# Performance work log

Measured on AMD Instinct MI355X. Metric: run time of the kernel, lower is better.

Reference implementation:

```python
import jax, jax.numpy as jnp
import numpy as np

NUM_ROUTES = 32 * 6 * 6  # 1152
NUM_CAPS = 10
IN_DIM = 8
OUT_DIM = 16
NUM_ITERS = 3

def _conv(x, w, stride):
    return jax.lax.conv_general_dilated(
        x, w, window_strides=(stride, stride), padding='VALID',
        dimension_numbers=('NCHW', 'OIHW', 'NCHW'))

def _squash(u):
    # squash over last axis, exactly as torch code (no eps)
    sn = (u ** 2).sum(-1, keepdims=True)
    return sn * u / ((1.0 + sn) * jnp.sqrt(sn))

def setup_inputs() -> dict:
    key = jax.random.key(0)
    ks = jax.random.split(key, 10)
    B = 512
    data = jax.random.normal(ks[0], (B, 1, 28, 28), dtype=jnp.float32)
    conv_w = jax.random.normal(ks[1], (256, 1, 9, 9), dtype=jnp.float32) * 0.05
    conv_b = jnp.zeros((256,), dtype=jnp.float32)
    # 8 primary-capsule convs stacked caps-major -> fused conv [8*32,256,9,9]
    pc_w = jax.random.normal(ks[2], (8 * 32, 256, 9, 9), dtype=jnp.float32) * 0.01
    pc_b = jnp.zeros((8 * 32,), dtype=jnp.float32)
    W = jax.random.normal(ks[3], (NUM_ROUTES, NUM_CAPS, OUT_DIM, IN_DIM), dtype=jnp.float32)
    enc_w1 = jax.random.normal(ks[4], (512, OUT_DIM * NUM_CAPS), dtype=jnp.float32) * 0.05
    enc_b1 = jnp.zeros((512,), dtype=jnp.float32)
    enc_w2 = jax.random.normal(ks[5], (9, 512), dtype=jnp.float32) * 0.05
    enc_b2 = jnp.zeros((9,), dtype=jnp.float32)
    return dict(data=data, conv_w=conv_w, conv_b=conv_b, pc_w=pc_w, pc_b=pc_b,
                W=W, enc_w1=enc_w1, enc_b1=enc_b1, enc_w2=enc_w2, enc_b2=enc_b2)

def reference(data, conv_w, conv_b, pc_w, pc_b, W, enc_w1, enc_b1, enc_w2, enc_b2):
    B = data.shape[0]
    # ConvLayer: conv + relu -> [B,256,20,20]
    x = jax.nn.relu(_conv(data, conv_w, 1) + conv_b[None, :, None, None])
    # PrimaryCaps: 8 stride-2 convs (fused, caps-major channels) -> [B,256,6,6]
    u = _conv(x, pc_w, 2) + pc_b[None, :, None, None]
    # torch: stack(dim=1) then view(B, num_routes, -1) == reshape caps-major flat
    u = u.reshape(B, NUM_ROUTES, IN_DIM)
    u = _squash(u)  # [B,R,8]
    # WaferCaps: u_hat[b,r,c,o] = sum_i W[r,c,o,i] * u[b,r,i]
    u_hat = jnp.einsum('rcoi,bri->brco', W, u)  # [B,R,C,O]
    b_ij = jnp.zeros((NUM_ROUTES, NUM_CAPS), dtype=u_hat.dtype)
    v = None
    for it in range(NUM_ITERS):
        c_ij = jax.nn.softmax(b_ij, axis=0)  # softmax over routes (dim=1 in torch)
        s = jnp.einsum('rc,brco->bco', c_ij, u_hat)  # [B,C,O]
        # original squashes [B,1,C,O,1] over last (size-1) dim -> elementwise
        s2 = s ** 2
        v = s2 * s / ((1.0 + s2) * jnp.sqrt(s2))  # = s*|s|/(1+s^2)
        if it < NUM_ITERS - 1:
            a = jnp.einsum('brco,bco->brc', u_hat, v)  # [B,R,C]
            b_ij = b_ij + a.mean(axis=0)
    # Encoder: flatten [B,C,O] row-major -> [B,160]
    flat = v.reshape(B, NUM_CAPS * OUT_DIM)
    h = jax.nn.relu(flat @ enc_w1.T + enc_b1)  # dropout is identity at eval
    out = jax.nn.sigmoid(h @ enc_w2.T + enc_b2)
    return out
```

## Files before the change

kernel.cpp:

```cpp
#include <hip/hip_runtime.h>
#include <hip/hip_bf16.h>
#include <stdint.h>


typedef __bf16 bf16_t;
typedef __bf16 bf16x4 __attribute__((ext_vector_type(4)));
typedef __bf16 bf16x8 __attribute__((ext_vector_type(8)));
typedef float f32x4 __attribute__((ext_vector_type(4)));
typedef int i32x4 __attribute__((ext_vector_type(4)));
typedef int i32x8 __attribute__((ext_vector_type(8)));

__device__ __forceinline__ void gload_lds16(const void* g, void* l) {
    __builtin_amdgcn_global_load_lds((const __attribute__((address_space(1))) void*)g,
                                     (__attribute__((address_space(3))) void*)l, 16, 0, 0);
}

#define MEMBAR() asm volatile("" ::: "memory")

__device__ __forceinline__ uint8_t fp8b(float v) {
    return (uint8_t)(__builtin_amdgcn_cvt_pk_fp8_f32(v, 0.f, 0, false) & 0xFF);
}

__global__ void k_prep(const float* __restrict__ w1, const float* __restrict__ cw,
                       float* __restrict__ w1t, bf16_t* __restrict__ Bc1,
                       float* __restrict__ bij) {
    int blk = blockIdx.x, tid = threadIdx.x;
    if (blk < 45) {
        int i = blk * 256 + tid;
        if (i < 11520) bij[i] = 0.f;
    } else if (blk < 365) {
        int i = (blk - 45) * 256 + tid;
        int j = i / 160, k = i % 160;
        w1t[k * 512 + j] = w1[i];
    } else {
        int i = (blk - 365) * 256 + tid;
        if (i < 26624) {
            int oc = i / 104, k = i % 104;
            Bc1[i] = (k < 81) ? (bf16_t)cw[oc * 81 + k] : (bf16_t)0.f;
        }
    }
}

__global__ __launch_bounds__(256) void k_w2t(const float* __restrict__ pcw,
                                             uint8_t* __restrict__ w2t8) {
    __shared__ uint16_t tmp16[10368];
    int oc = blockIdx.x, tid = threadIdx.x;
    const float* src = pcw + (size_t)oc * 20736;
    for (int q2 = tid; q2 < 10368; q2 += 256) {
        float a = src[q2 * 2] * 64.f;
        float b = src[q2 * 2 + 1] * 64.f;
        uint32_t pk = __builtin_amdgcn_cvt_pk_fp8_f32(a, b, 0, false);
        tmp16[q2] = (uint16_t)(pk & 0xFFFF);
    }
    __syncthreads();
    uint32_t* dst = (uint32_t*)(w2t8 + (size_t)oc * 20736);
    for (int w = tid; w < 5184; w += 256) {
        int k = w * 4;
        int t = k >> 8, ic0 = k & 255;
        uint32_t r = 0;
#pragma unroll
        for (int j = 0; j < 4; ++j) {
            int s = (ic0 + j) * 81 + t;
            uint32_t b = (tmp16[s >> 1] >> ((s & 1) * 8)) & 0xFF;
            r |= b << (8 * j);
        }
        dst[w] = r;
    }
}

__global__ __launch_bounds__(512) void k_c1gemm(const float* __restrict__ data,
                                                const bf16_t* __restrict__ Bc1,
                                                const float* __restrict__ cb,
                                                uint8_t* __restrict__ xt8) {
    __shared__ __align__(16) bf16_t As[128 * 104];
    __shared__ __align__(16) bf16_t Bs[256 * 104];
    int tid = threadIdx.x, lane = tid & 63, wave = tid >> 6;
    int wm = wave >> 2, wn = wave & 3;
    for (int i = tid; i < 3328; i += 512) {
        int byte = i * 16;
        int r = byte / 208;
        int c16 = (byte - r * 208) >> 4;
        gload_lds16(Bc1 + r * 104 + c16 * 8, (char*)Bs + byte);
    }
    int mr = wm * 64 + (lane & 15);
    int nr = wn * 64 + (lane & 15);
    float bias[4];
#pragma unroll
    for (int nj = 0; nj < 4; ++nj) bias[nj] = cb[nr + nj * 16];

    for (int t = 0; t < 2; ++t) {
        int m0 = (blockIdx.x + t * 800) * 128;
        __syncthreads();
        for (int z = tid; z < 128 * 23; z += 512) {
            int r = z / 23, k = 81 + z - (z / 23) * 23;
            As[r * 104 + k] = (bf16_t)0.f;
        }
        for (int pr = tid; pr < 1152; pr += 512) {
            int r = pr / 9, kh = pr - (pr / 9) * 9;
            int m = m0 + r;
            int b = m / 400, pos = m - b * 400;
            int oh = pos / 20, ow = pos - oh * 20;
            const float* src = data + (size_t)b * 784 + (oh + kh) * 28 + ow;
            bf16_t* dst = &As[r * 104 + kh * 9];
#pragma unroll
            for (int j = 0; j < 9; ++j) dst[j] = (bf16_t)src[j];
        }
        asm volatile("s_waitcnt vmcnt(0)" ::: "memory");
        __syncthreads();
        f32x4 acc[4][4];
#pragma unroll
        for (int mi = 0; mi < 4; ++mi)
#pragma unroll
            for (int nj = 0; nj < 4; ++nj) acc[mi][nj] = (f32x4){0.f, 0.f, 0.f, 0.f};
#pragma unroll
        for (int kk = 0; kk < 3; ++kk) {
            int ch = (kk * 4 + (lane >> 4)) * 8;
            bf16x8 af[4], bfr[4];
#pragma unroll
            for (int i = 0; i < 4; ++i) af[i] = *(const bf16x8*)&As[(mr + i * 16) * 104 + ch];
#pragma unroll
            for (int j = 0; j < 4; ++j) bfr[j] = *(const bf16x8*)&Bs[(nr + j * 16) * 104 + ch];
#pragma unroll
            for (int mi = 0; mi < 4; ++mi)
#pragma unroll
                for (int nj = 0; nj < 4; ++nj)
                    acc[mi][nj] = __builtin_amdgcn_mfma_f32_16x16x32_bf16(af[mi], bfr[nj], acc[mi][nj], 0, 0, 0);
        }
        int mbase = m0 + wm * 64 + (lane >> 4) * 4;
#pragma unroll
        for (int mi = 0; mi < 4; ++mi)
#pragma unroll
            for (int nj = 0; nj < 4; ++nj)
#pragma unroll
                for (int j = 0; j < 4; ++j)
                    xt8[(size_t)(mbase + mi * 16 + j) * 256 + nr + nj * 16] =
                        fp8b(fmaxf(acc[mi][nj][j] + bias[nj], 0.f));
    }
}

__global__ __launch_bounds__(256) void k_pcgemm(const uint8_t* __restrict__ xt8,
                                                const uint8_t* __restrict__ w2t8,
                                                bf16_t* __restrict__ parts) {
    __shared__ __align__(16) uint8_t As[128 * 128];
    __shared__ __align__(16) uint8_t Bs[128 * 128];
    int bid = blockIdx.x;
    int mt = bid % 144;
    int nt = (bid / 144) & 1;
    int ks = bid / 288;
    int m0 = mt * 128, n0 = nt * 128;
    int tid = threadIdx.x, lane = tid & 63, wave = tid >> 6;

    int csrc = (tid & 7) ^ ((tid >> 3) & 7);
    int arow[4];
#pragma unroll
    for (int p = 0; p < 4; ++p) {
        int m = m0 + p * 32 + (tid >> 3);
        int bb = m / 36, pos = m % 36;
        int oh = pos / 6, ow = pos % 6;
        arow[p] = ((bb * 20 + oh * 2) * 20 + ow * 2) * 256;
    }
    const uint8_t* bbase = w2t8 + (size_t)(n0 + (tid >> 3)) * 20736 + csrc * 16;

    f32x4 acc[4][4];
#pragma unroll
    for (int mi = 0; mi < 4; ++mi)
#pragma unroll
        for (int ni = 0; ni < 4; ++ni) acc[mi][ni] = (f32x4){0.f, 0.f, 0.f, 0.f};

    int g0 = ks * 81;
    int mr = (wave >> 1) * 64 + (lane & 15);
    int nr = (wave & 1) * 64 + (lane & 15);
    int rx = lane & 7;
    int c0 = (2 * (lane >> 4)) ^ rx;
    int c1 = (2 * (lane >> 4) + 1) ^ rx;

    for (int it = 0; it < 81; ++it) {
        int g = g0 + it;
        int t = g >> 1, icb = g & 1;
        int kh = t / 9, kw = t - (t / 9) * 9;
        int aoff = (kh * 20 + kw) * 256 + icb * 128 + csrc * 16;
#pragma unroll
        for (int p = 0; p < 4; ++p) {
            gload_lds16(xt8 + arow[p] + aoff, &As[p * 4096 + tid * 16]);
            gload_lds16(bbase + (size_t)p * 32 * 20736 + (size_t)g * 128, &Bs[p * 4096 + tid * 16]);
        }
        __syncthreads();
        i32x8 af[4], bfr[4];
#pragma unroll
        for (int i = 0; i < 4; ++i) {
            i32x4 lo = *(const i32x4*)&As[(mr + i * 16) * 128 + c0 * 16];
            i32x4 hi = *(const i32x4*)&As[(mr + i * 16) * 128 + c1 * 16];
            af[i][0] = lo[0]; af[i][1] = lo[1]; af[i][2] = lo[2]; af[i][3] = lo[3];
            af[i][4] = hi[0]; af[i][5] = hi[1]; af[i][6] = hi[2]; af[i][7] = hi[3];
        }
#pragma unroll
        for (int i = 0; i < 4; ++i) {
            i32x4 lo = *(const i32x4*)&Bs[(nr + i * 16) * 128 + c0 * 16];
            i32x4 hi = *(const i32x4*)&Bs[(nr + i * 16) * 128 + c1 * 16];
            bfr[i][0] = lo[0]; bfr[i][1] = lo[1]; bfr[i][2] = lo[2]; bfr[i][3] = lo[3];
            bfr[i][4] = hi[0]; bfr[i][5] = hi[1]; bfr[i][6] = hi[2]; bfr[i][7] = hi[3];
        }
#pragma unroll
        for (int mi = 0; mi < 4; ++mi)
#pragma unroll
            for (int ni = 0; ni < 4; ++ni)
                acc[mi][ni] = __builtin_amdgcn_mfma_scale_f32_16x16x128_f8f6f4(
                    af[mi], bfr[ni], acc[mi][ni], 0, 0, 0, 0x7F7F7F7F, 0, 0x79797979);
        __syncthreads();
    }

    bf16_t* out = parts + (size_t)ks * 4718592;
    int mbase = m0 + (wave >> 1) * 64 + (lane >> 4) * 4;
    int nbase = n0 + (wave & 1) * 64 + (lane & 15);
#pragma unroll
    for (int mi = 0; mi < 4; ++mi)
#pragma unroll
        for (int ni = 0; ni < 4; ++ni)
#pragma unroll
            for (int j = 0; j < 4; ++j)
                out[(size_t)(mbase + mi * 16 + j) * 256 + nbase + ni * 16] = (bf16_t)acc[mi][ni][j];
}

__global__ __launch_bounds__(256) void k_squash(const bf16_t* __restrict__ parts,
                                                const float* __restrict__ pcb,
                                                bf16_t* __restrict__ ub) {
    __shared__ float s[36 * 257];
    int b = blockIdx.x, tid = threadIdx.x;
    for (int i = tid; i < 9216; i += 256) {
        float a = pcb[i & 255];
#pragma unroll
        for (int p = 0; p < 2; ++p) a += (float)parts[(size_t)p * 4718592 + (size_t)b * 9216 + i];
        s[(i >> 8) * 257 + (i & 255)] = a;
    }
    __syncthreads();
    for (int r = tid; r < 1152; r += 256) {
        int flat0 = r * 8;
        float val[8], sn = 0.f;
#pragma unroll
        for (int e = 0; e < 8; ++e) {
            int f = flat0 + e;
            float x = s[(f % 36) * 257 + f / 36];
            val[e] = x;
            sn += x * x;
        }
        float scale = sn / ((1.f + sn) * sqrtf(sn));
        bf16x8 vv;
#pragma unroll
        for (int e = 0; e < 8; ++e) vv[e] = (bf16_t)(val[e] * scale);
        *(bf16x8*)&ub[(size_t)b * 9216 + flat0] = vv;
    }
}

__global__ __launch_bounds__(256) void k_uT(const bf16_t* __restrict__ ub, bf16_t* __restrict__ uT) {
    __shared__ bf16_t t[64 * 66];
    int kt = blockIdx.x % 144, bt = blockIdx.x / 144;
    int k0 = kt * 64, b0 = bt * 64;
    int tid = threadIdx.x;
    int c8 = tid & 7;
#pragma unroll
    for (int p = 0; p < 2; ++p) {
        int r = p * 32 + (tid >> 3);
        bf16x8 vv = *(const bf16x8*)&ub[(size_t)(b0 + r) * 9216 + k0 + c8 * 8];
        uint32_t u4[4];
        *(bf16x8*)u4 = vv;
#pragma unroll
        for (int j2 = 0; j2 < 4; ++j2)
            *(uint32_t*)&t[r * 66 + c8 * 8 + j2 * 2] = u4[j2];
    }
    __syncthreads();
#pragma unroll
    for (int p = 0; p < 2; ++p) {
        int kp = p * 32 + (tid >> 3);
        bf16x8 vv;
#pragma unroll
        for (int j = 0; j < 8; ++j) vv[j] = t[(c8 * 8 + j) * 66 + kp];
        *(bf16x8*)&uT[(size_t)(k0 + kp) * 512 + b0 + c8 * 8] = vv;
    }
}

__global__ void k_cij(const float* __restrict__ bij, float* __restrict__ cij) {
    __shared__ float red[256];
    int c = blockIdx.x, tid = threadIdx.x;
    float mx = -1e30f;
    for (int r = tid; r < 1152; r += 256) mx = fmaxf(mx, bij[r * 10 + c]);
    red[tid] = mx; __syncthreads();
    for (int s = 128; s > 0; s >>= 1) { if (tid < s) red[tid] = fmaxf(red[tid], red[tid + s]); __syncthreads(); }
    float MX = red[0]; __syncthreads();
    float sm = 0.f;
    for (int r = tid; r < 1152; r += 256) sm += expf(bij[r * 10 + c] - MX);
    red[tid] = sm; __syncthreads();
    for (int s = 128; s > 0; s >>= 1) { if (tid < s) red[tid] += red[tid + s]; __syncthreads(); }
    float inv = 1.f / red[0];
    for (int r = tid; r < 1152; r += 256) cij[r * 10 + c] = expf(bij[r * 10 + c] - MX) * inv;
}

__global__ void k_fold(const float* __restrict__ cij, const float* __restrict__ W,
                       bf16_t* __restrict__ cw2T) {
    int idx = blockIdx.x * 256 + threadIdx.x;
    int co = idx / 9216, k = idx % 9216;
    int r = k >> 3, i = k & 7;
    int c = co >> 4, o = co & 15;
    cw2T[idx] = (bf16_t)(cij[r * 10 + c] * W[((size_t)(r * 10 + c) * 16 + o) * 8 + i]);
}

__global__ void k_fold0(const float* __restrict__ W, bf16_t* __restrict__ cw2T) {
    int idx = blockIdx.x * 256 + threadIdx.x;
    int co = idx / 9216, k = idx % 9216;
    int r = k >> 3, i = k & 7;
    int c = co >> 4, o = co & 15;
    cw2T[idx] = (bf16_t)(W[((size_t)(r * 10 + c) * 16 + o) * 8 + i] * (1.0f / 1152.0f));
}

__global__ __launch_bounds__(256) void k_rgemm(const bf16_t* __restrict__ A,
                                               const bf16_t* __restrict__ B,
                                               bf16_t* __restrict__ Cp,
                                               int Kfull, int steps, int mtiles) {
    __shared__ __align__(16) bf16_t As[64 * 64];
    __shared__ __align__(16) bf16_t Bs[160 * 64];
    int bid = blockIdx.x;
    int mt = bid % mtiles, ks = bid / mtiles;
    int m0 = mt * 64;
    int k0 = ks * steps * 64;
    int tid = threadIdx.x, lane = tid & 63, wave = tid >> 6;
    int srow = tid >> 3;
    int csrc = (tid & 7) ^ (srow & 7);
    const bf16_t* asrc[2];
    const bf16_t* bsrc[5];
#pragma unroll
    for (int p = 0; p < 2; ++p)
        asrc[p] = A + (size_t)(m0 + p * 32 + srow) * Kfull + k0 + csrc * 8;
#pragma unroll
    for (int p = 0; p < 5; ++p)
        bsrc[p] = B + (size_t)(p * 32 + srow) * Kfull + k0 + csrc * 8;

    f32x4 acc[2][5];
#pragma unroll
    for (int mi = 0; mi < 2; ++mi)
#pragma unroll
        for (int nj = 0; nj < 5; ++nj) acc[mi][nj] = (f32x4){0.f, 0.f, 0.f, 0.f};

    int mr = (wave >> 1) * 32 + (lane & 15);
    int nr = (wave & 1) * 80 + (lane & 15);
    int rx = lane & 7;

    for (int it = 0; it < steps; ++it) {
#pragma unroll
        for (int p = 0; p < 2; ++p) gload_lds16(asrc[p] + it * 64, As + p * 2048 + tid * 8);
#pragma unroll
        for (int p = 0; p < 5; ++p) gload_lds16(bsrc[p] + it * 64, Bs + p * 2048 + tid * 8);
        __syncthreads();
#pragma unroll
        for (int kk = 0; kk < 2; ++kk) {
            int ch = ((kk * 4 + (lane >> 4)) ^ rx) * 8;
            bf16x8 af[2], bfr[5];
#pragma unroll
            for (int i = 0; i < 2; ++i) af[i] = *(const bf16x8*)&As[(mr + i * 16) * 64 + ch];
#pragma unroll
            for (int j = 0; j < 5; ++j) bfr[j] = *(const bf16x8*)&Bs[(nr + j * 16) * 64 + ch];
#pragma unroll
            for (int mi = 0; mi < 2; ++mi)
#pragma unroll
                for (int nj = 0; nj < 5; ++nj)
                    acc[mi][nj] = __builtin_amdgcn_mfma_f32_16x16x32_bf16(af[mi], bfr[nj], acc[mi][nj], 0, 0, 0);
        }
        __syncthreads();
    }

    bf16_t* out = Cp + (size_t)ks * ((size_t)mtiles * 64 * 160);
    int mbase = m0 + (wave >> 1) * 32 + (lane >> 4) * 4;
    int nbase = (wave & 1) * 80 + (lane & 15);
#pragma unroll
    for (int mi = 0; mi < 2; ++mi)
#pragma unroll
        for (int nj = 0; nj < 5; ++nj)
#pragma unroll
            for (int j = 0; j < 4; ++j)
                out[(size_t)(mbase + mi * 16 + j) * 160 + nbase + nj * 16] = (bf16_t)acc[mi][nj][j];
}

__global__ void k_vcomp(const bf16_t* __restrict__ sp, float* __restrict__ v,
                        bf16_t* __restrict__ vT) {
    int idx = blockIdx.x * 256 + threadIdx.x;
    float s = 0.f;
#pragma unroll
    for (int p = 0; p < 36; ++p) s += (float)sp[(size_t)p * 81920 + idx];
    float val = s * fabsf(s) / (1.f + s * s);
    v[idx] = val;
    int b = idx / 160, co = idx % 160;
    vT[(size_t)co * 512 + b] = (bf16_t)val;
}

__global__ __launch_bounds__(256) void k_ggemm2(const bf16_t* __restrict__ uT,
                                                const bf16_t* __restrict__ vT,
                                                const float* __restrict__ W,
                                                float* __restrict__ bij) {
    __shared__ __align__(16) bf16_t As[64 * 64];
    __shared__ __align__(16) bf16_t Bs[160 * 64];
    __shared__ float Gl[64 * 161];
    int mt = blockIdx.x;
    int m0 = mt * 64;
    int tid = threadIdx.x, lane = tid & 63, wave = tid >> 6;
    int srow = tid >> 3;
    int csrc = (tid & 7) ^ (srow & 7);
    const bf16_t* asrc[2];
    const bf16_t* bsrc[5];
#pragma unroll
    for (int p = 0; p < 2; ++p)
        asrc[p] = uT + (size_t)(m0 + p * 32 + srow) * 512 + csrc * 8;
#pragma unroll
    for (int p = 0; p < 5; ++p)
        bsrc[p] = vT + (size_t)(p * 32 + srow) * 512 + csrc * 8;

    f32x4 acc[2][5];
#pragma unroll
    for (int mi = 0; mi < 2; ++mi)
#pragma unroll
        for (int nj = 0; nj < 5; ++nj) acc[mi][nj] = (f32x4){0.f, 0.f, 0.f, 0.f};

    int mr = (wave >> 1) * 32 + (lane & 15);
    int nr = (wave & 1) * 80 + (lane & 15);
    int rx = lane & 7;

    for (int it = 0; it < 8; ++it) {
#pragma unroll
        for (int p = 0; p < 2; ++p) gload_lds16(asrc[p] + it * 64, As + p * 2048 + tid * 8);
#pragma unroll
        for (int p = 0; p < 5; ++p) gload_lds16(bsrc[p] + it * 64, Bs + p * 2048 + tid * 8);
        __syncthreads();
#pragma unroll
        for (int kk = 0; kk < 2; ++kk) {
            int ch = ((kk * 4 + (lane >> 4)) ^ rx) * 8;
            bf16x8 af[2], bfr[5];
#pragma unroll
            for (int i = 0; i < 2; ++i) af[i] = *(const bf16x8*)&As[(mr + i * 16) * 64 + ch];
#pragma unroll
            for (int j = 0; j < 5; ++j) bfr[j] = *(const bf16x8*)&Bs[(nr + j * 16) * 64 + ch];
#pragma unroll
            for (int mi = 0; mi < 2; ++mi)
#pragma unroll
                for (int nj = 0; nj < 5; ++nj)
                    acc[mi][nj] = __builtin_amdgcn_mfma_f32_16x16x32_bf16(af[mi], bfr[nj], acc[mi][nj], 0, 0, 0);
        }
        __syncthreads();
    }

    int mbl = (wave >> 1) * 32 + (lane >> 4) * 4;
    int nbase = (wave & 1) * 80 + (lane & 15);
#pragma unroll
    for (int mi = 0; mi < 2; ++mi)
#pragma unroll
        for (int nj = 0; nj < 5; ++nj)
#pragma unroll
            for (int j = 0; j < 4; ++j)
                Gl[(mbl + mi * 16 + j) * 161 + nbase + nj * 16] = acc[mi][nj][j] * (1.0f / 512.0f);
    __syncthreads();
    if (tid < 80) {
        int rl = tid / 10, c = tid % 10;
        int r = mt * 8 + rl;
        const float* wbase = W + (size_t)(r * 10 + c) * 128;
        float s = 0.f;
#pragma unroll
        for (int o = 0; o < 16; ++o)
#pragma unroll
            for (int i = 0; i < 8; ++i)
                s += wbase[o * 8 + i] * Gl[(rl * 8 + i) * 161 + c * 16 + o];
        bij[r * 10 + c] += s;
    }
}

__global__ __launch_bounds__(256) void k_enc(const float* __restrict__ v,
                                             const float* __restrict__ w1t,
                                             const float* __restrict__ b1,
                                             const float* __restrict__ w2,
                                             const float* __restrict__ b2,
                                             float* __restrict__ out) {
    __shared__ float fl[160];
    __shared__ float h[512];
    int b = blockIdx.x, tid = threadIdx.x;
    if (tid < 160) fl[tid] = v[b * 160 + tid];
    __syncthreads();
    for (int j = tid; j < 512; j += 256) {
        float s = b1[j];
#pragma unroll 8
        for (int k = 0; k < 160; ++k) s += fl[k] * w1t[k * 512 + j];
        h[j] = fmaxf(s, 0.f);
    }
    __syncthreads();
    int wave = tid >> 6, lane = tid & 63;
    for (int j = wave; j < 9; j += 4) {
        float p = 0.f;
#pragma unroll
        for (int l = lane; l < 512; l += 64) p += h[l] * w2[j * 512 + l];
#pragma unroll
        for (int off = 32; off > 0; off >>= 1) p += __shfl_down(p, off, 64);
        if (lane == 0) out[b * 9 + j] = 1.f / (1.f + expf(-(p + b2[j])));
    }
}

extern "C" void kernel_launch(void* const* d_in, const int* in_sizes, int n_in,
                              void* d_out, int out_size, void* d_ws, size_t ws_size,
                              hipStream_t stream) {
    const float* data   = (const float*)d_in[0];
    const float* conv_w = (const float*)d_in[1];
    const float* conv_b = (const float*)d_in[2];
    const float* pc_w   = (const float*)d_in[3];
    const float* pc_b   = (const float*)d_in[4];
    const float* W      = (const float*)d_in[5];
    const float* enc_w1 = (const float*)d_in[6];
    const float* enc_b1 = (const float*)d_in[7];
    const float* enc_w2 = (const float*)d_in[8];
    const float* enc_b2 = (const float*)d_in[9];

    char* ws = (char*)d_ws;
    uint8_t* xt8   = (uint8_t*)(ws + 0);
    uint8_t* w2t8  = (uint8_t*)(ws + 52428800);
    bf16_t*  parts = (bf16_t*)(ws + 57737216);
    bf16_t*  uT    = (bf16_t*)(ws + 76611584);
    bf16_t*  cw2T  = (bf16_t*)(ws + 86048768);
    bf16_t*  sp    = (bf16_t*)(ws + 88997888);
    bf16_t*  ub    = (bf16_t*)(ws + 94896128);
    float*   v     = (float*)(ws + 104333312);
    bf16_t*  vT    = (bf16_t*)(ws + 104660992);
    float*   w1t   = (float*)(ws + 104824832);
    float*   bij   = (float*)(ws + 105152512);
    float*   cij   = (float*)(ws + 105198592);
    bf16_t*  Bc1   = (bf16_t*)(ws + 105244672);
    float*   outp  = (float*)d_out;

    hipLaunchKernelGGL(k_prep, dim3(469), dim3(256), 0, stream, enc_w1, conv_w, w1t, Bc1, bij);
    hipLaunchKernelGGL(k_w2t, dim3(256), dim3(256), 0, stream, pc_w, w2t8);
    hipLaunchKernelGGL(k_c1gemm, dim3(800), dim3(512), 0, stream, data, Bc1, conv_b, xt8);
    hipLaunchKernelGGL(k_pcgemm, dim3(576), dim3(256), 0, stream, xt8, w2t8, parts);
    hipLaunchKernelGGL(k_squash, dim3(512), dim3(256), 0, stream, parts, pc_b, ub);
    hipLaunchKernelGGL(k_uT, dim3(1152), dim3(256), 0, stream, ub, uT);
    for (int it = 0; it < 3; ++it) {
        if (it == 0) {
            hipLaunchKernelGGL(k_fold0, dim3(5760), dim3(256), 0, stream, W, cw2T);
        } else {
            hipLaunchKernelGGL(k_cij, dim3(10), dim3(256), 0, stream, bij, cij);
            hipLaunchKernelGGL(k_fold, dim3(5760), dim3(256), 0, stream, cij, W, cw2T);
        }
        hipLaunchKernelGGL(k_rgemm, dim3(288), dim3(256), 0, stream, ub, cw2T, sp, 9216, 4, 8);
        hipLaunchKernelGGL(k_vcomp, dim3(320), dim3(256), 0, stream, sp, v, vT);
        if (it < 2) {
            hipLaunchKernelGGL(k_ggemm2, dim3(144), dim3(256), 0, stream, uT, vT, W, bij);
        }
    }
    hipLaunchKernelGGL(k_enc, dim3(512), dim3(256), 0, stream, v, w1t, enc_b1, enc_w2, enc_b2, outp);
}
```

Measured before the change: 286.5 us.

## Merge prep kernels, split GEMMs into more blocks, batch encoder rows

Folds the fp8 weight-transpose kernel into the prep kernel to save a launch. The conv1 GEMM now processes one tile per block across twice as many blocks. The primary-caps GEMM uses 64-wide N tiles, doubling its grid. The routing GEMM doubles its K-split, so the v reduction sums 72 partials, and the workspace offsets are shifted to fit the larger buffer. The encoder computes four batch rows per block so each w1 load is reused across rows; this trades larger grids and more partial sums for better occupancy.

```diff
diff --git a/kernel.cpp b/kernel.cpp
--- a/kernel.cpp
+++ b/kernel.cpp
@@ -21,9 +21,14 @@
     return (uint8_t)(__builtin_amdgcn_cvt_pk_fp8_f32(v, 0.f, 0, false) & 0xFF);
 }
 
-__global__ void k_prep(const float* __restrict__ w1, const float* __restrict__ cw,
-                       float* __restrict__ w1t, bf16_t* __restrict__ Bc1,
-                       float* __restrict__ bij) {
+__global__ __launch_bounds__(256) void k_prep(const float* __restrict__ w1,
+                                              const float* __restrict__ cw,
+                                              const float* __restrict__ pcw,
+                                              float* __restrict__ w1t,
+                                              bf16_t* __restrict__ Bc1,
+                                              float* __restrict__ bij,
+                                              uint8_t* __restrict__ w2t8) {
+    __shared__ uint16_t tmp16[10368];
     int blk = blockIdx.x, tid = threadIdx.x;
     if (blk < 45) {
         int i = blk * 256 + tid;
@@ -32,39 +37,35 @@
         int i = (blk - 45) * 256 + tid;
         int j = i / 160, k = i % 160;
         w1t[k * 512 + j] = w1[i];
-    } else {
+    } else if (blk < 469) {
         int i = (blk - 365) * 256 + tid;
         if (i < 26624) {
             int oc = i / 104, k = i % 104;
             Bc1[i] = (k < 81) ? (bf16_t)cw[oc * 81 + k] : (bf16_t)0.f;
         }
-    }
-}
-
-__global__ __launch_bounds__(256) void k_w2t(const float* __restrict__ pcw,
-                                             uint8_t* __restrict__ w2t8) {
-    __shared__ uint16_t tmp16[10368];
-    int oc = blockIdx.x, tid = threadIdx.x;
-    const float* src = pcw + (size_t)oc * 20736;
-    for (int q2 = tid; q2 < 10368; q2 += 256) {
-        float a = src[q2 * 2] * 64.f;
-        float b = src[q2 * 2 + 1] * 64.f;
-        uint32_t pk = __builtin_amdgcn_cvt_pk_fp8_f32(a, b, 0, false);
-        tmp16[q2] = (uint16_t)(pk & 0xFFFF);
-    }
-    __syncthreads();
-    uint32_t* dst = (uint32_t*)(w2t8 + (size_t)oc * 20736);
-    for (int w = tid; w < 5184; w += 256) {
-        int k = w * 4;
-        int t = k >> 8, ic0 = k & 255;
-        uint32_t r = 0;
-#pragma unroll
-        for (int j = 0; j < 4; ++j) {
-            int s = (ic0 + j) * 81 + t;
-            uint32_t b = (tmp16[s >> 1] >> ((s & 1) * 8)) & 0xFF;
-            r |= b << (8 * j);
-        }
-        dst[w] = r;
+    } else {
+        int oc = blk - 469;
+        const float* src = pcw + (size_t)oc * 20736;
+        for (int q2 = tid; q2 < 10368; q2 += 256) {
+            float a = src[q2 * 2] * 64.f;
+            float b = src[q2 * 2 + 1] * 64.f;
+            uint32_t pk = __builtin_amdgcn_cvt_pk_fp8_f32(a, b, 0, false);
+            tmp16[q2] = (uint16_t)(pk & 0xFFFF);
+        }
+        __syncthreads();
+        uint32_t* dst = (uint32_t*)(w2t8 + (size_t)oc * 20736);
+        for (int w = tid; w < 5184; w += 256) {
+            int k = w * 4;
+            int t = k >> 8, ic0 = k & 255;
+            uint32_t r = 0;
+#pragma unroll
+            for (int j = 0; j < 4; ++j) {
+                int s = (ic0 + j) * 81 + t;
+                uint32_t b = (tmp16[s >> 1] >> ((s & 1) * 8)) & 0xFF;
+                r |= b << (8 * j);
+            }
+            dst[w] = r;
+        }
     }
 }
 
@@ -88,66 +89,63 @@
 #pragma unroll
     for (int nj = 0; nj < 4; ++nj) bias[nj] = cb[nr + nj * 16];
 
-    for (int t = 0; t < 2; ++t) {
-        int m0 = (blockIdx.x + t * 800) * 128;
-        __syncthreads();
-        for (int z = tid; z < 128 * 23; z += 512) {
-            int r = z / 23, k = 81 + z - (z / 23) * 23;
-            As[r * 104 + k] = (bf16_t)0.f;
-        }
-        for (int pr = tid; pr < 1152; pr += 512) {
-            int r = pr / 9, kh = pr - (pr / 9) * 9;
-            int m = m0 + r;
-            int b = m / 400, pos = m - b * 400;
-            int oh = pos / 20, ow = pos - oh * 20;
-            const float* src = data + (size_t)b * 784 + (oh + kh) * 28 + ow;
-            bf16_t* dst = &As[r * 104 + kh * 9];
-#pragma unroll
-            for (int j = 0; j < 9; ++j) dst[j] = (bf16_t)src[j];
-        }
-        asm volatile("s_waitcnt vmcnt(0)" ::: "memory");
-        __syncthreads();
-        f32x4 acc[4][4];
+    int m0 = blockIdx.x * 128;
+    for (int z = tid; z < 128 * 23; z += 512) {
+        int r = z / 23, k = 81 + z - (z / 23) * 23;
+        As[r * 104 + k] = (bf16_t)0.f;
+    }
+    for (int pr = tid; pr < 1152; pr += 512) {
+        int r = pr / 9, kh = pr - (pr / 9) * 9;
+        int m = m0 + r;
+        int b = m / 400, pos = m - b * 400;
+        int oh = pos / 20, ow = pos - oh * 20;
+        const float* src = data + (size_t)b * 784 + (oh + kh) * 28 + ow;
+        bf16_t* dst = &As[r * 104 + kh * 9];
+#pragma unroll
+        for (int j = 0; j < 9; ++j) dst[j] = (bf16_t)src[j];
+    }
+    asm volatile("s_waitcnt vmcnt(0)" ::: "memory");
+    __syncthreads();
+    f32x4 acc[4][4];
+#pragma unroll
+    for (int mi = 0; mi < 4; ++mi)
+#pragma unroll
+        for (int nj = 0; nj < 4; ++nj) acc[mi][nj] = (f32x4){0.f, 0.f, 0.f, 0.f};
+#pragma unroll
+    for (int kk = 0; kk < 3; ++kk) {
+        int ch = (kk * 4 + (lane >> 4)) * 8;
+        bf16x8 af[4], bfr[4];
+#pragma unroll
+        for (int i = 0; i < 4; ++i) af[i] = *(const bf16x8*)&As[(mr + i * 16) * 104 + ch];
+#pragma unroll
+        for (int j = 0; j < 4; ++j) bfr[j] = *(const bf16x8*)&Bs[(nr + j * 16) * 104 + ch];
 #pragma unroll
         for (int mi = 0; mi < 4; ++mi)
 #pragma unroll
-            for (int nj = 0; nj < 4; ++nj) acc[mi][nj] = (f32x4){0.f, 0.f, 0.f, 0.f};
-#pragma unroll
-        for (int kk = 0; kk < 3; ++kk) {
-            int ch = (kk * 4 + (lane >> 4)) * 8;
-            bf16x8 af[4], bfr[4];
-#pragma unroll
-            for (int i = 0; i < 4; ++i) af[i] = *(const bf16x8*)&As[(mr + i * 16) * 104 + ch];
-#pragma unroll
-            for (int j = 0; j < 4; ++j) bfr[j] = *(const bf16x8*)&Bs[(nr + j * 16) * 104 + ch];
-#pragma unroll
-            for (int mi = 0; mi < 4; ++mi)
-#pragma unroll
-                for (int nj = 0; nj < 4; ++nj)
-                    acc[mi][nj] = __builtin_amdgcn_mfma_f32_16x16x32_bf16(af[mi], bfr[nj], acc[mi][nj], 0, 0, 0);
-        }
-        int mbase = m0 + wm * 64 + (lane >> 4) * 4;
-#pragma unroll
-        for (int mi = 0; mi < 4; ++mi)
-#pragma unroll
             for (int nj = 0; nj < 4; ++nj)
-#pragma unroll
-                for (int j = 0; j < 4; ++j)
-                    xt8[(size_t)(mbase + mi * 16 + j) * 256 + nr + nj * 16] =
-                        fp8b(fmaxf(acc[mi][nj][j] + bias[nj], 0.f));
-    }
+                acc[mi][nj] = __builtin_amdgcn_mfma_f32_16x16x32_bf16(af[mi], bfr[nj], acc[mi][nj], 0, 0, 0);
+    }
+    int mbase = m0 + wm * 64 + (lane >> 4) * 4;
+#pragma unroll
+    for (int mi = 0; mi < 4; ++mi)
+#pragma unroll
+        for (int nj = 0; nj < 4; ++nj)
+#pragma unroll
+            for (int j = 0; j < 4; ++j)
+                xt8[(size_t)(mbase + mi * 16 + j) * 256 + nr + nj * 16] =
+                    fp8b(fmaxf(acc[mi][nj][j] + bias[nj], 0.f));
 }
 
 __global__ __launch_bounds__(256) void k_pcgemm(const uint8_t* __restrict__ xt8,
                                                 const uint8_t* __restrict__ w2t8,
                                                 bf16_t* __restrict__ parts) {
     __shared__ __align__(16) uint8_t As[128 * 128];
-    __shared__ __align__(16) uint8_t Bs[128 * 128];
+    __shared__ __align__(16) uint8_t Bs[64 * 128];
     int bid = blockIdx.x;
     int mt = bid % 144;
-    int nt = (bid / 144) & 1;
-    int ks = bid / 288;
-    int m0 = mt * 128, n0 = nt * 128;
+    int nt = (bid / 144) & 3;
+    int ks = bid / 576;
+    int m0 = mt * 128, n0 = nt * 64;
     int tid = threadIdx.x, lane = tid & 63, wave = tid >> 6;
 
     int csrc = (tid & 7) ^ ((tid >> 3) & 7);
@@ -161,15 +159,15 @@
     }
     const uint8_t* bbase = w2t8 + (size_t)(n0 + (tid >> 3)) * 20736 + csrc * 16;
 
-    f32x4 acc[4][4];
+    f32x4 acc[4][2];
 #pragma unroll
     for (int mi = 0; mi < 4; ++mi)
 #pragma unroll
-        for (int ni = 0; ni < 4; ++ni) acc[mi][ni] = (f32x4){0.f, 0.f, 0.f, 0.f};
+        for (int ni = 0; ni < 2; ++ni) acc[mi][ni] = (f32x4){0.f, 0.f, 0.f, 0.f};
 
     int g0 = ks * 81;
     int mr = (wave >> 1) * 64 + (lane & 15);
-    int nr = (wave & 1) * 64 + (lane & 15);
+    int nr = (wave & 1) * 32 + (lane & 15);
     int rx = lane & 7;
     int c0 = (2 * (lane >> 4)) ^ rx;
     int c1 = (2 * (lane >> 4) + 1) ^ rx;
@@ -180,12 +178,13 @@
         int kh = t / 9, kw = t - (t / 9) * 9;
         int aoff = (kh * 20 + kw) * 256 + icb * 128 + csrc * 16;
 #pragma unroll
-        for (int p = 0; p < 4; ++p) {
+        for (int p = 0; p < 4; ++p)
             gload_lds16(xt8 + arow[p] + aoff, &As[p * 4096 + tid * 16]);
+#pragma unroll
+        for (int p = 0; p < 2; ++p)
             gload_lds16(bbase + (size_t)p * 32 * 20736 + (size_t)g * 128, &Bs[p * 4096 + tid * 16]);
-        }
-        __syncthreads();
-        i32x8 af[4], bfr[4];
+        __syncthreads();
+        i32x8 af[4], bfr[2];
 #pragma unroll
         for (int i = 0; i < 4; ++i) {
             i32x4 lo = *(const i32x4*)&As[(mr + i * 16) * 128 + c0 * 16];
@@ -194,7 +193,7 @@
             af[i][4] = hi[0]; af[i][5] = hi[1]; af[i][6] = hi[2]; af[i][7] = hi[3];
         }
 #pragma unroll
-        for (int i = 0; i < 4; ++i) {
+        for (int i = 0; i < 2; ++i) {
             i32x4 lo = *(const i32x4*)&Bs[(nr + i * 16) * 128 + c0 * 16];
             i32x4 hi = *(const i32x4*)&Bs[(nr + i * 16) * 128 + c1 * 16];
             bfr[i][0] = lo[0]; bfr[i][1] = lo[1]; bfr[i][2] = lo[2]; bfr[i][3] = lo[3];
@@ -203,7 +202,7 @@
 #pragma unroll
         for (int mi = 0; mi < 4; ++mi)
 #pragma unroll
-            for (int ni = 0; ni < 4; ++ni)
+            for (int ni = 0; ni < 2; ++ni)
                 acc[mi][ni] = __builtin_amdgcn_mfma_scale_f32_16x16x128_f8f6f4(
                     af[mi], bfr[ni], acc[mi][ni], 0, 0, 0, 0x7F7F7F7F, 0, 0x79797979);
         __syncthreads();
@@ -211,11 +210,11 @@
 
     bf16_t* out = parts + (size_t)ks * 4718592;
     int mbase = m0 + (wave >> 1) * 64 + (lane >> 4) * 4;
-    int nbase = n0 + (wave & 1) * 64 + (lane & 15);
+    int nbase = n0 + (wave & 1) * 32 + (lane & 15);
 #pragma unroll
     for (int mi = 0; mi < 4; ++mi)
 #pragma unroll
-        for (int ni = 0; ni < 4; ++ni)
+        for (int ni = 0; ni < 2; ++ni)
 #pragma unroll
             for (int j = 0; j < 4; ++j)
                 out[(size_t)(mbase + mi * 16 + j) * 256 + nbase + ni * 16] = (bf16_t)acc[mi][ni][j];
@@ -382,8 +381,7 @@
                         bf16_t* __restrict__ vT) {
     int idx = blockIdx.x * 256 + threadIdx.x;
     float s = 0.f;
-#pragma unroll
-    for (int p = 0; p < 36; ++p) s += (float)sp[(size_t)p * 81920 + idx];
+    for (int p = 0; p < 72; ++p) s += (float)sp[(size_t)p * 81920 + idx];
     float val = s * fabsf(s) / (1.f + s * s);
     v[idx] = val;
     int b = idx / 160, co = idx % 160;
@@ -474,26 +472,36 @@
                                              const float* __restrict__ w2,
                                              const float* __restrict__ b2,
                                              float* __restrict__ out) {
-    __shared__ float fl[160];
-    __shared__ float h[512];
-    int b = blockIdx.x, tid = threadIdx.x;
-    if (tid < 160) fl[tid] = v[b * 160 + tid];
+    __shared__ float fl[4 * 160];
+    __shared__ float h[4 * 512];
+    int b0 = blockIdx.x * 4, tid = threadIdx.x;
+    for (int i = tid; i < 640; i += 256) fl[i] = v[(size_t)b0 * 160 + i];
     __syncthreads();
     for (int j = tid; j < 512; j += 256) {
-        float s = b1[j];
-#pragma unroll 8
-        for (int k = 0; k < 160; ++k) s += fl[k] * w1t[k * 512 + j];
-        h[j] = fmaxf(s, 0.f);
+        float bb = b1[j];
+        float a0 = bb, a1 = bb, a2 = bb, a3 = bb;
+        for (int k = 0; k < 160; ++k) {
+            float w = w1t[k * 512 + j];
+            a0 += fl[k] * w;
+            a1 += fl[160 + k] * w;
+            a2 += fl[320 + k] * w;
+            a3 += fl[480 + k] * w;
+        }
+        h[j] = fmaxf(a0, 0.f);
+        h[512 + j] = fmaxf(a1, 0.f);
+        h[1024 + j] = fmaxf(a2, 0.f);
+        h[1536 + j] = fmaxf(a3, 0.f);
     }
     __syncthreads();
     int wave = tid >> 6, lane = tid & 63;
-    for (int j = wave; j < 9; j += 4) {
+    int q = wave;
+    for (int j = 0; j < 9; ++j) {
         float p = 0.f;
 #pragma unroll
-        for (int l = lane; l < 512; l += 64) p += h[l] * w2[j * 512 + l];
+        for (int l = lane; l < 512; l += 64) p += h[q * 512 + l] * w2[j * 512 + l];
 #pragma unroll
         for (int off = 32; off > 0; off >>= 1) p += __shfl_down(p, off, 64);
-        if (lane == 0) out[b * 9 + j] = 1.f / (1.f + expf(-(p + b2[j])));
+        if (lane == 0) out[(b0 + q) * 9 + j] = 1.f / (1.f + expf(-(p + b2[j])));
     }
 }
 
@@ -518,19 +526,18 @@
     bf16_t*  uT    = (bf16_t*)(ws + 76611584);
     bf16_t*  cw2T  = (bf16_t*)(ws + 86048768);
     bf16_t*  sp    = (bf16_t*)(ws + 88997888);
-    bf16_t*  ub    = (bf16_t*)(ws + 94896128);
-    float*   v     = (float*)(ws + 104333312);
-    bf16_t*  vT    = (bf16_t*)(ws + 104660992);
-    float*   w1t   = (float*)(ws + 104824832);
-    float*   bij   = (float*)(ws + 105152512);
-    float*   cij   = (float*)(ws + 105198592);
-    bf16_t*  Bc1   = (bf16_t*)(ws + 105244672);
+    bf16_t*  ub    = (bf16_t*)(ws + 100794368);
+    float*   v     = (float*)(ws + 110231552);
+    bf16_t*  vT    = (bf16_t*)(ws + 110559232);
+    float*   w1t   = (float*)(ws + 110723072);
+    float*   bij   = (float*)(ws + 111050752);
+    float*   cij   = (float*)(ws + 111096832);
+    bf16_t*  Bc1   = (bf16_t*)(ws + 111142912);
     float*   outp  = (float*)d_out;
 
-    hipLaunchKernelGGL(k_prep, dim3(469), dim3(256), 0, stream, enc_w1, conv_w, w1t, Bc1, bij);
-    hipLaunchKernelGGL(k_w2t, dim3(256), dim3(256), 0, stream, pc_w, w2t8);
-    hipLaunchKernelGGL(k_c1gemm, dim3(800), dim3(512), 0, stream, data, Bc1, conv_b, xt8);
-    hipLaunchKernelGGL(k_pcgemm, dim3(576), dim3(256), 0, stream, xt8, w2t8, parts);
+    hipLaunchKernelGGL(k_prep, dim3(725), dim3(256), 0, stream, enc_w1, conv_w, pc_w, w1t, Bc1, bij, w2t8);
+    hipLaunchKernelGGL(k_c1gemm, dim3(1600), dim3(512), 0, stream, data, Bc1, conv_b, xt8);
+    hipLaunchKernelGGL(k_pcgemm, dim3(1152), dim3(256), 0, stream, xt8, w2t8, parts);
     hipLaunchKernelGGL(k_squash, dim3(512), dim3(256), 0, stream, parts, pc_b, ub);
     hipLaunchKernelGGL(k_uT, dim3(1152), dim3(256), 0, stream, ub, uT);
     for (int it = 0; it < 3; ++it) {
@@ -540,11 +547,11 @@
             hipLaunchKernelGGL(k_cij, dim3(10), dim3(256), 0, stream, bij, cij);
             hipLaunchKernelGGL(k_fold, dim3(5760), dim3(256), 0, stream, cij, W, cw2T);
         }
-        hipLaunchKernelGGL(k_rgemm, dim3(288), dim3(256), 0, stream, ub, cw2T, sp, 9216, 4, 8);
+        hipLaunchKernelGGL(k_rgemm, dim3(576), dim3(256), 0, stream, ub, cw2T, sp, 9216, 2, 8);
         hipLaunchKernelGGL(k_vcomp, dim3(320), dim3(256), 0, stream, sp, v, vT);
         if (it < 2) {
             hipLaunchKernelGGL(k_ggemm2, dim3(144), dim3(256), 0, stream, uT, vT, W, bij);
         }
     }
-    hipLaunchKernelGGL(k_enc, dim3(512), dim3(256), 0, stream, v, w1t, enc_b1, enc_w2, enc_b2, outp);
-}
+    hipLaunchKernelGGL(k_enc, dim3(128), dim3(256), 0, stream, v, w1t, enc_b1, enc_w2, enc_b2, outp);
+}
```

Result: slower. 293.4 us (+2.4%).
